# Performance work log

Measured on AMD Instinct MI355X. Metric: run time of the kernel, lower is better.

## Reference

```python
import jax, jax.numpy as jnp
import numpy as np

B, V, CODE_NUM = 64, 100, 4096
CODE_SIZE, ATT, VISIT, TIME, HID, OUT = 256, 128, 256, 64, 512, 90
TYPE_NUM = 32
NEG = -2.0 ** 31


def setup_inputs() -> dict:
    key = jax.random.key(0)
    ks = jax.random.split(key, 24)
    s = 0.02
    return {
        'code_x': jax.random.randint(ks[0], (B, V, CODE_NUM), 0, 2).astype(jnp.float32),
        'code_type0': jax.random.randint(ks[1], (CODE_NUM + 1,), 0, TYPE_NUM),
        'code_type1': jax.random.randint(ks[2], (CODE_NUM + 1,), 0, TYPE_NUM),
        'code_type2': jax.random.randint(ks[3], (CODE_NUM + 1,), 0, TYPE_NUM),
        'lens': jax.random.randint(ks[4], (B,), 1, V + 1),
        'intervals': jax.random.uniform(ks[5], (B, V), dtype=jnp.float32),
        # encoder: code + 3 type embedding tables (rows 1..code_num used)
        'code_emb': jax.random.normal(ks[6], (CODE_NUM + 1, CODE_SIZE), jnp.float32) * s,
        't0_emb': jax.random.normal(ks[7], (TYPE_NUM, CODE_SIZE), jnp.float32) * s,
        't1_emb': jax.random.normal(ks[8], (TYPE_NUM, CODE_SIZE), jnp.float32) * s,
        't2_emb': jax.random.normal(ks[9], (TYPE_NUM, CODE_SIZE), jnp.float32) * s,
        # visit self-attention (no bias, per nn.Linear(..., bias=False))
        'Wq': jax.random.normal(ks[10], (CODE_SIZE, ATT), jnp.float32) * s,
        'Wk': jax.random.normal(ks[11], (CODE_SIZE, ATT), jnp.float32) * s,
        'Wv': jax.random.normal(ks[12], (CODE_SIZE, VISIT), jnp.float32) * s,
        # time embedding Linear(1, time_size)
        'time_w': jax.random.normal(ks[13], (TIME,), jnp.float32) * s,
        'time_b': jnp.zeros((TIME,), jnp.float32),
        # GRUCell params (torch layout: gates ordered r,z,n)
        'gru_Wih': jax.random.normal(ks[14], (3 * HID, VISIT + TIME), jnp.float32) * s,
        'gru_Whh': jax.random.normal(ks[15], (3 * HID, HID), jnp.float32) * s,
        'gru_bih': jnp.zeros((3 * HID,), jnp.float32),
        'gru_bhh': jnp.zeros((3 * HID,), jnp.float32),
        # classifier
        'cls_W': jax.random.normal(ks[16], (OUT, HID), jnp.float32) * s,
        'cls_b': jnp.zeros((OUT,), jnp.float32),
    }


def reference(code_x, code_type0, code_type1, code_type2, lens, intervals,
              code_emb, t0_emb, t1_emb, t2_emb, Wq, Wk, Wv, time_w, time_b,
              gru_Wih, gru_Whh, gru_bih, gru_bhh, cls_W, cls_b):
    # --- Encoder (vectorized): multi-hot slot i corresponds to code id i+1 ---
    E = (code_emb[1:]
         + t0_emb[code_type0[1:]]
         + t1_emb[code_type1[1:]]
         + t2_emb[code_type2[1:]])                      # [CODE_NUM, CODE_SIZE]
    active = (code_x > 0).astype(E.dtype)               # [B, V, CODE_NUM]
    counts = jnp.maximum(active.sum(-1, keepdims=True), 1.0)
    v_emb_ini = jnp.einsum('bvc,cd->bvd', active, E) / counts  # mean over codes
    visit_mask = jnp.arange(V)[None, :] < lens[:, None]        # [B, V]
    v_emb_ini = v_emb_ini * visit_mask[..., None]              # padded visits stay 0

    # --- Context-aware visit self-attention ---
    Q = v_emb_ini @ Wq                                   # [B, V, ATT]
    K = v_emb_ini @ Wk
    Vv = v_emb_ini @ Wv                                  # [B, V, VISIT]
    alpha = jnp.einsum('bqa,bka->bqk', Q, K)
    alpha = jnp.where(visit_mask[:, None, :], alpha, NEG)  # mask keys
    alpha = jax.nn.softmax(alpha, axis=2)
    v_emb = jnp.einsum('bqk,bkd->bqd', alpha, Vv) + Vv     # [B, V, VISIT]

    # --- Time-aware input ---
    t_emb = intervals[..., None] * time_w + time_b         # [B, V, TIME]
    x = jnp.concatenate([v_emb, t_emb], axis=-1)           # [B, V, VISIT+TIME]

    # --- GRU over visits, gated by per-patient length ---
    def step(h, xm):
        xt, mt = xm                                        # xt [B,D], mt [B]
        gi = xt @ gru_Wih.T + gru_bih
        gh = h @ gru_Whh.T + gru_bhh
        ir, iz, inn = jnp.split(gi, 3, axis=-1)
        hr, hz, hn = jnp.split(gh, 3, axis=-1)
        r = jax.nn.sigmoid(ir + hr)
        z = jax.nn.sigmoid(iz + hz)
        n = jnp.tanh(inn + r * hn)
        h_new = (1.0 - z) * n + z * h
        h = jnp.where(mt[:, None], h_new, h)
        return h, None

    h0 = jnp.zeros((B, HID), x.dtype)
    h_final, _ = jax.lax.scan(step, h0, (x.transpose(1, 0, 2), visit_mask.T))

    # --- Classifier (dropout p=0 -> identity) ---
    return jax.nn.sigmoid(h_final @ cls_W.T + cls_b)       # [B, OUT]
```

## Files before the change

kernel.cpp:

```cpp
#include <hip/hip_runtime.h>
#include <hip/hip_bf16.h>

typedef float  f32x4 __attribute__((ext_vector_type(4)));
typedef short  s16x8 __attribute__((ext_vector_type(8)));

#define NEGBIG -1e30f

__device__ __forceinline__ unsigned short f2b(float f) {
    union { float f; unsigned u; } c; c.f = f;
    unsigned r = c.u + 0x7FFF + ((c.u >> 16) & 1);
    return (unsigned short)(r >> 16);
}
__device__ __forceinline__ float b2f(unsigned short h) {
    union { unsigned u; float f; } c; c.u = ((unsigned)h) << 16;
    return c.f;
}
__device__ __forceinline__ float sigm(float x) { return 1.f / (1.f + __expf(-x)); }

__device__ __forceinline__ s16x8 ld_b128_sc(const unsigned short* p) {
    s16x8 r;
    asm volatile("global_load_dwordx4 %0, %1, off sc0 sc1" : "=v"(r) : "v"(p));
    return r;
}
__device__ __forceinline__ void st_short_sc(unsigned short* p, unsigned short v) {
    unsigned int dv = v;
    asm volatile("global_store_short %0, %1, off sc0 sc1" :: "v"(p), "v"(dv) : "memory");
}
__device__ __forceinline__ void st_dword_sc(float* p, float v) {
    asm volatile("global_store_dword %0, %1, off sc0 sc1" :: "v"(p), "v"(v) : "memory");
}

__global__ __launch_bounds__(256) void prep_all(const float* code_emb, const int* ct0, const int* ct1, const int* ct2,
                                                const float* t0e, const float* t1e, const float* t2e,
                                                const float* Wq, const float* Wk, const float* Wv,
                                                const float* gWih, const float* gWhh,
                                                unsigned short* ET, unsigned short* wcat,
                                                unsigned short* wih, unsigned short* whh,
                                                int* flags, unsigned short* hb0) {
    __shared__ float tile[64][65];
    const int bid = blockIdx.x;
    const int t = threadIdx.x;
    if (bid < 256) {
        const int d0 = (bid & 3) * 64, c0 = (bid >> 2) * 64;
        for (int p = 0; p < 16; ++p) {
            int idx = p * 256 + t;
            int dl = idx & 63, cl = idx >> 6;
            int code = c0 + cl + 1;
            int d = d0 + dl;
            float v = code_emb[code * 256 + d] + t0e[ct0[code] * 256 + d]
                    + t1e[ct1[code] * 256 + d] + t2e[ct2[code] * 256 + d];
            tile[dl][cl] = v;
        }
        __syncthreads();
        for (int p = 0; p < 2; ++p) {
            int idx = p * 256 + t;
            int dl = idx >> 3, ch = idx & 7;
            s16x8 pk;
#pragma unroll
            for (int e = 0; e < 8; ++e) pk[e] = (short)f2b(tile[dl][ch * 8 + e]);
            *(s16x8*)(ET + (size_t)(d0 + dl) * 4096 + c0 + ch * 8) = pk;
        }
    } else {
        if (bid >= 504) {
            int idx = (bid - 504) * 256 + t;
            for (int i = idx; i < 1024; i += 2048) flags[i] = 0;
            for (int i = idx; i < 32768; i += 2048) hb0[i] = 0;
        }
        int idx = (bid - 256) * 256 + t;
        const int stride = 256 * 256;
        const int N1 = 131072, N2 = 491520, N3 = 786432;
        for (; idx < N1 + N2 + N3; idx += stride) {
            if (idx < N1) {
                int n = idx >> 8, k = idx & 255;
                float v;
                if (n < 128) v = Wq[k * 128 + n];
                else if (n < 256) v = Wk[k * 128 + (n - 128)];
                else v = Wv[k * 256 + (n - 256)];
                wcat[n * 256 + k] = f2b(v);
            } else if (idx < N1 + N2) {
                int i = idx - N1; wih[i] = f2b(gWih[i]);
            } else {
                int i = idx - N1 - N2; whh[i] = f2b(gWhh[i]);
            }
        }
    }
}

__global__ __launch_bounds__(256) void enc_gemm(const float* code_x, const unsigned short* ET,
                                                const int* lens, unsigned short* Vb) {
    __shared__ __align__(16) char sm[4096 + 32768 + 128];
    char* As = sm;
    char* Bs = sm + 4096;
    float* cl = (float*)(sm + 4096 + 32768);
    const int m0 = blockIdx.x * 32;
    const int t = threadIdx.x, l = t & 63, w = t >> 6;
    const int lr = l & 15, lq = l >> 4, l7 = l & 7;
    const int sr = t >> 3, sc = t & 7;
    const int bn = t >> 3, bc = t & 7;
    const float* gabase = code_x + (size_t)(m0 + sr) * 4096 + sc * 8;
    f32x4 acc[2][4];
#pragma unroll
    for (int a = 0; a < 2; ++a)
#pragma unroll
        for (int b = 0; b < 4; ++b) acc[a][b] = (f32x4){0.f, 0.f, 0.f, 0.f};
    int cnt = 0;

    f32x4 a0A, a1A, a0B, a1B;
    s16x8 bA[8], bB[8];

#define ENC_ISSUE(SLOT, IT) do {                                                     \
    const int k0_ = (IT) * 64;                                                       \
    a0##SLOT = *(const f32x4*)(gabase + k0_);                                        \
    a1##SLOT = *(const f32x4*)(gabase + k0_ + 4);                                    \
    _Pragma("unroll")                                                                \
    for (int rd_ = 0; rd_ < 8; ++rd_)                                                \
        b##SLOT[rd_] = *(const s16x8*)(ET + (size_t)(rd_ * 32 + bn) * 4096 + k0_ + bc * 8); \
} while (0)

#define ENC_CONSUME(SLOT, NEXTIT) do {                                               \
    s16x8 ap_;                                                                       \
    _Pragma("unroll")                                                                \
    for (int e_ = 0; e_ < 4; ++e_) { bool on_ = a0##SLOT[e_] > 0.f; ap_[e_] = on_ ? (short)0x3F80 : (short)0; cnt += on_ ? 1 : 0; } \
    _Pragma("unroll")                                                                \
    for (int e_ = 0; e_ < 4; ++e_) { bool on_ = a1##SLOT[e_] > 0.f; ap_[4 + e_] = on_ ? (short)0x3F80 : (short)0; cnt += on_ ? 1 : 0; } \
    *(s16x8*)(As + sr * 128 + ((sc ^ (sr & 7)) << 4)) = ap_;                         \
    _Pragma("unroll")                                                                \
    for (int rd_ = 0; rd_ < 8; ++rd_) {                                              \
        int n_ = rd_ * 32 + bn;                                                      \
        *(s16x8*)(Bs + n_ * 128 + ((bc ^ (n_ & 7)) << 4)) = b##SLOT[rd_];            \
    }                                                                                \
    if ((NEXTIT) < 64) ENC_ISSUE(SLOT, NEXTIT);                                      \
    __syncthreads();                                                                 \
    _Pragma("unroll")                                                                \
    for (int kk_ = 0; kk_ < 2; ++kk_) {                                              \
        const int cp_ = kk_ * 4 + lq;                                                \
        s16x8 af_[2], bf_[4];                                                        \
        _Pragma("unroll")                                                            \
        for (int mt_ = 0; mt_ < 2; ++mt_)                                            \
            af_[mt_] = *(const s16x8*)(As + (mt_ * 16 + lr) * 128 + ((cp_ ^ l7) << 4)); \
        _Pragma("unroll")                                                            \
        for (int nt_ = 0; nt_ < 4; ++nt_)                                            \
            bf_[nt_] = *(const s16x8*)(Bs + ((w * 4 + nt_) * 16 + lr) * 128 + ((cp_ ^ l7) << 4)); \
        _Pragma("unroll")                                                            \
        for (int mt_ = 0; mt_ < 2; ++mt_)                                            \
            _Pragma("unroll")                                                        \
            for (int nt_ = 0; nt_ < 4; ++nt_)                                        \
                acc[mt_][nt_] = __builtin_amdgcn_mfma_f32_16x16x32_bf16(af_[mt_], bf_[nt_], acc[mt_][nt_], 0, 0, 0); \
    }                                                                                \
    __syncthreads();                                                                 \
} while (0)

    ENC_ISSUE(A, 0);
    ENC_ISSUE(B, 1);
    for (int base = 0; base < 64; base += 2) {
        ENC_CONSUME(A, base + 2);
        ENC_CONSUME(B, base + 3);
    }
#undef ENC_ISSUE
#undef ENC_CONSUME

    float fc = (float)cnt;
    fc += __shfl_xor(fc, 1); fc += __shfl_xor(fc, 2); fc += __shfl_xor(fc, 4);
    if (sc == 0) cl[sr] = fmaxf(fc, 1.f);
    __syncthreads();
#pragma unroll
    for (int mt = 0; mt < 2; ++mt)
#pragma unroll
        for (int i = 0; i < 4; ++i) {
            int m = mt * 16 + lq * 4 + i;
            int gm = m0 + m;
            float rc = 1.f / cl[m];
            unsigned bi = (unsigned)gm / 100u;
            unsigned vi = (unsigned)gm - bi * 100u;
            float msk = ((int)vi < lens[bi]) ? 1.f : 0.f;
#pragma unroll
            for (int nt = 0; nt < 4; ++nt) {
                int n = (w * 4 + nt) * 16 + lr;
                Vb[(size_t)gm * 256 + n] = f2b(acc[mt][nt][i] * rc * msk);
            }
        }
}

__global__ __launch_bounds__(256) void gemm_bf16(const unsigned short* A, const unsigned short* Bm,
                                                 int K, int Ntot, int mode,
                                                 unsigned short* outp, const float* bias) {
    __shared__ __align__(16) char sm[4096 + 32768];
    char* As = sm;
    char* Bs = sm + 4096;
    const int m0 = blockIdx.x * 32;
    const int n0 = blockIdx.y * 256;
    const int t = threadIdx.x, l = t & 63, w = t >> 6;
    const int lr = l & 15, lq = l >> 4, l7 = l & 7;
    const int sr = t >> 3, sc = t & 7;
    const int bn = t >> 3, bc = t & 7;
    const int iters = K >> 6;
    f32x4 acc[2][4];
#pragma unroll
    for (int a = 0; a < 2; ++a)
#pragma unroll
        for (int b = 0; b < 4; ++b) acc[a][b] = (f32x4){0.f, 0.f, 0.f, 0.f};

    s16x8 avA, avB;
    s16x8 bA[8], bB[8];

#define GB_ISSUE(SLOT, IT) do {                                                      \
    const int k0_ = (IT) * 64;                                                       \
    av##SLOT = *(const s16x8*)(A + (size_t)(m0 + sr) * K + k0_ + sc * 8);            \
    _Pragma("unroll")                                                                \
    for (int rd_ = 0; rd_ < 8; ++rd_)                                                \
        b##SLOT[rd_] = *(const s16x8*)(Bm + (size_t)(n0 + rd_ * 32 + bn) * K + k0_ + bc * 8); \
} while (0)

#define GB_CONSUME(SLOT, NEXTIT) do {                                                \
    *(s16x8*)(As + sr * 128 + ((sc ^ (sr & 7)) << 4)) = av##SLOT;                    \
    _Pragma("unroll")                                                                \
    for (int rd_ = 0; rd_ < 8; ++rd_) {                                              \
        int n_ = rd_ * 32 + bn;                                                      \
        *(s16x8*)(Bs + n_ * 128 + ((bc ^ (n_ & 7)) << 4)) = b##SLOT[rd_];            \
    }                                                                                \
    if ((NEXTIT) < iters) GB_ISSUE(SLOT, NEXTIT);                                    \
    __syncthreads();                                                                 \
    _Pragma("unroll")                                                                \
    for (int kk_ = 0; kk_ < 2; ++kk_) {                                              \
        const int cp_ = kk_ * 4 + lq;                                                \
        s16x8 af_[2], bf_[4];                                                        \
        _Pragma("unroll")                                                            \
        for (int mt_ = 0; mt_ < 2; ++mt_)                                            \
            af_[mt_] = *(const s16x8*)(As + (mt_ * 16 + lr) * 128 + ((cp_ ^ l7) << 4)); \
        _Pragma("unroll")                                                            \
        for (int nt_ = 0; nt_ < 4; ++nt_)                                            \
            bf_[nt_] = *(const s16x8*)(Bs + ((w * 4 + nt_) * 16 + lr) * 128 + ((cp_ ^ l7) << 4)); \
        _Pragma("unroll")                                                            \
        for (int mt_ = 0; mt_ < 2; ++mt_)                                            \
            _Pragma("unroll")                                                        \
            for (int nt_ = 0; nt_ < 4; ++nt_)                                        \
                acc[mt_][nt_] = __builtin_amdgcn_mfma_f32_16x16x32_bf16(af_[mt_], bf_[nt_], acc[mt_][nt_], 0, 0, 0); \
    }                                                                                \
    __syncthreads();                                                                 \
} while (0)

    GB_ISSUE(A, 0);
    if (iters > 1) GB_ISSUE(B, 1);
    for (int base = 0; base < iters; base += 2) {
        GB_CONSUME(A, base + 2);
        if (base + 1 < iters) GB_CONSUME(B, base + 3);
    }
#undef GB_ISSUE
#undef GB_CONSUME

#pragma unroll
    for (int mt = 0; mt < 2; ++mt)
#pragma unroll
        for (int i = 0; i < 4; ++i) {
            int gm = m0 + mt * 16 + lq * 4 + i;
#pragma unroll
            for (int nt = 0; nt < 4; ++nt) {
                int n = n0 + (w * 4 + nt) * 16 + lr;
                float v = acc[mt][nt][i];
                if (mode == 1) v += bias[n];
                outp[(size_t)gm * Ntot + n] = f2b(v);
            }
        }
}

__global__ __launch_bounds__(256) void attn_kernel(const unsigned short* QKV, const int* lens,
                                                   const float* intervals, const float* time_w, const float* time_b,
                                                   unsigned short* X) {
    __shared__ __align__(16) char sm[28672 + 32768];
    char* Pb = sm;
    char* VTb = sm + 28672;
    const int b = blockIdx.x;
    const int h = blockIdx.y;
    const int t = threadIdx.x, l = t & 63, w = t >> 6;
    const int lr = l & 15, lq = l >> 4;
    const int lenb = lens[b];
    for (int p = 0; p < 7; ++p) {
        int idx = p * 256 + t;
        *(f32x4*)(Pb + idx * 16) = (f32x4){0.f, 0.f, 0.f, 0.f};
    }
    __syncthreads();
    f32x4 S[2][7];
#pragma unroll
    for (int a = 0; a < 2; ++a)
#pragma unroll
        for (int c = 0; c < 7; ++c) S[a][c] = (f32x4){0.f, 0.f, 0.f, 0.f};
#pragma unroll
    for (int kk = 0; kk < 4; ++kk) {
        s16x8 qa[2], kb[7];
#pragma unroll
        for (int mi = 0; mi < 2; ++mi) {
            int mt = 2 * w + mi;
            if (mt > 6) continue;
            int row = b * 100 + mt * 16 + lr;
            qa[mi] = *(const s16x8*)(QKV + (size_t)row * 512 + kk * 32 + lq * 8);
        }
#pragma unroll
        for (int nt = 0; nt < 7; ++nt) {
            int row = b * 100 + nt * 16 + lr;
            kb[nt] = *(const s16x8*)(QKV + (size_t)row * 512 + 128 + kk * 32 + lq * 8);
        }
#pragma unroll
        for (int mi = 0; mi < 2; ++mi) {
            int mt = 2 * w + mi;
            if (mt > 6) continue;
#pragma unroll
            for (int nt = 0; nt < 7; ++nt)
                S[mi][nt] = __builtin_amdgcn_mfma_f32_16x16x32_bf16(qa[mi], kb[nt], S[mi][nt], 0, 0, 0);
        }
    }
#pragma unroll
    for (int mi = 0; mi < 2; ++mi) {
        int mt = 2 * w + mi;
        if (mt > 6) continue;
        float sv[7][4];
#pragma unroll
        for (int nt = 0; nt < 7; ++nt) {
            int j = nt * 16 + lr;
#pragma unroll
            for (int i = 0; i < 4; ++i)
                sv[nt][i] = (j < lenb) ? S[mi][nt][i] : NEGBIG;
        }
#pragma unroll
        for (int i = 0; i < 4; ++i) {
            float mx = sv[0][i];
#pragma unroll
            for (int nt = 1; nt < 7; ++nt) mx = fmaxf(mx, sv[nt][i]);
            mx = fmaxf(mx, __shfl_xor(mx, 1));
            mx = fmaxf(mx, __shfl_xor(mx, 2));
            mx = fmaxf(mx, __shfl_xor(mx, 4));
            mx = fmaxf(mx, __shfl_xor(mx, 8));
            float e[7], sum = 0.f;
#pragma unroll
            for (int nt = 0; nt < 7; ++nt) { e[nt] = __expf(sv[nt][i] - mx); sum += e[nt]; }
            sum += __shfl_xor(sum, 1);
            sum += __shfl_xor(sum, 2);
            sum += __shfl_xor(sum, 4);
            sum += __shfl_xor(sum, 8);
            float rs = 1.f / sum;
            int m = mt * 16 + lq * 4 + i;
#pragma unroll
            for (int nt = 0; nt < 7; ++nt) {
                int j = nt * 16 + lr;
                *(unsigned short*)(Pb + m * 256 + (((j >> 3) ^ (m & 7)) << 4) + ((j & 7) << 1)) = f2b(e[nt] * rs);
            }
        }
    }
    __syncthreads();
    for (int p = 0; p < 8; ++p) {
        int idx = p * 256 + t;
        *(f32x4*)(VTb + idx * 16) = (f32x4){0.f, 0.f, 0.f, 0.f};
    }
    __syncthreads();
    for (int p = 0; p < 7; ++p) {
        int ci = p * 256 + t;
        if (ci < 1600) {
            int j = ci >> 4, d8 = ci & 15;
            s16x8 vv = *(const s16x8*)(QKV + (size_t)(b * 100 + j) * 512 + 256 + h * 128 + d8 * 8);
#pragma unroll
            for (int e = 0; e < 8; ++e) {
                int dl = d8 * 8 + e;
                *(unsigned short*)(VTb + dl * 256 + (((j >> 3) ^ (dl & 7)) << 4) + ((j & 7) << 1)) = (unsigned short)vv[e];
            }
        }
    }
    __syncthreads();
    f32x4 O[2][8];
#pragma unroll
    for (int a = 0; a < 2; ++a)
#pragma unroll
        for (int c = 0; c < 8; ++c) O[a][c] = (f32x4){0.f, 0.f, 0.f, 0.f};
#pragma unroll
    for (int kk = 0; kk < 4; ++kk) {
        s16x8 pa[2];
#pragma unroll
        for (int mi = 0; mi < 2; ++mi) {
            int mt = 2 * w + mi;
            if (mt > 6) continue;
            int m = mt * 16 + lr;
            pa[mi] = *(const s16x8*)(Pb + m * 256 + (((kk * 4 + lq) ^ (m & 7)) << 4));
        }
#pragma unroll
        for (int nt = 0; nt < 8; ++nt) {
            int dl = nt * 16 + lr;
            s16x8 vb = *(const s16x8*)(VTb + dl * 256 + (((kk * 4 + lq) ^ (dl & 7)) << 4));
#pragma unroll
            for (int mi = 0; mi < 2; ++mi) {
                int mt = 2 * w + mi;
                if (mt > 6) continue;
                O[mi][nt] = __builtin_amdgcn_mfma_f32_16x16x32_bf16(pa[mi], vb, O[mi][nt], 0, 0, 0);
            }
        }
    }
#pragma unroll
    for (int mi = 0; mi < 2; ++mi) {
        int mt = 2 * w + mi;
        if (mt > 6) continue;
#pragma unroll
        for (int i = 0; i < 4; ++i) {
            int m = mt * 16 + lq * 4 + i;
            if (m < 100) {
#pragma unroll
                for (int nt = 0; nt < 8; ++nt) {
                    int dl = nt * 16 + lr;
                    float res = b2f(*(unsigned short*)(VTb + dl * 256 + (((m >> 3) ^ (dl & 7)) << 4) + ((m & 7) << 1)));
                    X[(size_t)(b * 100 + m) * 320 + h * 128 + dl] = f2b(O[mi][nt][i] + res);
                }
            }
        }
    }
    if (h == 0) {
        for (int p = 0; p < 25; ++p) {
            int idx = p * 256 + t;
            int m = idx >> 6, d = idx & 63;
            float val = intervals[b * 100 + m] * time_w[d] + time_b[d];
            X[(size_t)(b * 100 + m) * 320 + 256 + d] = f2b(val);
        }
    }
}

__global__ __launch_bounds__(256, 1) void gru_kernel(const unsigned short* GIb, const unsigned short* WHH,
                                                     const float* gbhh, const int* lens,
                                                     unsigned short* hb0, unsigned short* hb1, float* hf,
                                                     int* flags, const float* clsW, const float* clsb, float* out) {
    const int bid = blockIdx.x;
    const int t = threadIdx.x, l = t & 63, w = t >> 6;
    const int lr = l & 15, lq = l >> 4;
    const int d0 = bid * 16;
    const int j = d0 + lr;
    int ml;
    {
        int v = lens[l];
        v = max(v, __shfl_xor(v, 1));  v = max(v, __shfl_xor(v, 2));
        v = max(v, __shfl_xor(v, 4));  v = max(v, __shfl_xor(v, 8));
        v = max(v, __shfl_xor(v, 16)); v = max(v, __shfl_xor(v, 32));
        ml = v;
    }
    int lens4[4];
#pragma unroll
    for (int i = 0; i < 4; ++i) lens4[i] = lens[w * 16 + lq * 4 + i];
    const float bhr = gbhh[j], bhz = gbhh[512 + j], bhn = gbhh[1024 + j];
    s16x8 Bf[3][16];
#pragma unroll
    for (int g = 0; g < 3; ++g)
#pragma unroll
        for (int kk = 0; kk < 16; ++kk)
            Bf[g][kk] = *(const s16x8*)(WHH + (size_t)(g * 512 + j) * 512 + kk * 32 + lq * 8);
    float ho[4] = {0.f, 0.f, 0.f, 0.f};
    size_t gi_base[4];
#pragma unroll
    for (int i = 0; i < 4; ++i) gi_base[i] = (size_t)((w * 16 + lq * 4 + i) * 100) * 1536 + j;

    float gir[4], giz[4], gin[4];
#pragma unroll
    for (int i = 0; i < 4; ++i) {
        const unsigned short* gp = GIb + gi_base[i];
        gir[i] = b2f(gp[0]); giz[i] = b2f(gp[512]); gin[i] = b2f(gp[1024]);
    }

    for (int step = 0; step < ml; ++step) {
        const unsigned short* hb = (step & 1) ? hb1 : hb0;
        unsigned short* hn = (step & 1) ? hb0 : hb1;
        s16x8 af[16];
#pragma unroll
        for (int kk = 0; kk < 16; ++kk)
            af[kk] = ld_b128_sc(hb + (size_t)(w * 16 + lr) * 512 + kk * 32 + lq * 8);
        asm volatile("s_waitcnt vmcnt(0)" ::: "memory");
        __builtin_amdgcn_sched_barrier(0);
        f32x4 ar = (f32x4){0.f,0.f,0.f,0.f}, az = ar, an = ar;
#pragma unroll
        for (int kk = 0; kk < 16; ++kk) {
            ar = __builtin_amdgcn_mfma_f32_16x16x32_bf16(af[kk], Bf[0][kk], ar, 0, 0, 0);
            az = __builtin_amdgcn_mfma_f32_16x16x32_bf16(af[kk], Bf[1][kk], az, 0, 0, 0);
            an = __builtin_amdgcn_mfma_f32_16x16x32_bf16(af[kk], Bf[2][kk], an, 0, 0, 0);
        }
#pragma unroll
        for (int i = 0; i < 4; ++i) {
            float r = sigm(gir[i] + ar[i] + bhr);
            float z = sigm(giz[i] + az[i] + bhz);
            float n = tanhf(gin[i] + r * (an[i] + bhn));
            float hv = (step < lens4[i]) ? ((1.f - z) * n + z * ho[i]) : ho[i];
            ho[i] = hv;
            st_short_sc(hn + (size_t)(w * 16 + lq * 4 + i) * 512 + j, f2b(hv));
        }
        asm volatile("s_waitcnt vmcnt(0)" ::: "memory");
        __syncthreads();
        if (t == 0)
            __hip_atomic_store(flags + bid * 16, step + 1, __ATOMIC_RELAXED, __HIP_MEMORY_SCOPE_AGENT);
        if (step + 1 < ml) {
#pragma unroll
            for (int i = 0; i < 4; ++i) {
                const unsigned short* gp = GIb + gi_base[i] + (size_t)(step + 1) * 1536;
                gir[i] = b2f(gp[0]); giz[i] = b2f(gp[512]); gin[i] = b2f(gp[1024]);
            }
        }
        if (w == 0) {
            int guard = 0;
            while (true) {
                int v = (l < 32) ? __hip_atomic_load(flags + l * 16, __ATOMIC_RELAXED, __HIP_MEMORY_SCOPE_AGENT) : (step + 1);
                if (__all(v >= step + 1)) break;
                if (++guard > (1 << 20)) break;
                __builtin_amdgcn_s_sleep(1);
            }
        }
        __syncthreads();
    }
#pragma unroll
    for (int i = 0; i < 4; ++i)
        st_dword_sc(hf + (size_t)(w * 16 + lq * 4 + i) * 512 + j, ho[i]);
    asm volatile("s_waitcnt vmcnt(0)" ::: "memory");
    __syncthreads();
    if (t == 0)
        __hip_atomic_store(flags + bid * 16, ml + 1, __ATOMIC_RELAXED, __HIP_MEMORY_SCOPE_AGENT);
    if (w == 0) {
        int guard = 0;
        while (true) {
            int v = (l < 32) ? __hip_atomic_load(flags + l * 16, __ATOMIC_RELAXED, __HIP_MEMORY_SCOPE_AGENT) : (ml + 1);
            if (__all(v >= ml + 1)) break;
            if (++guard > (1 << 20)) break;
            __builtin_amdgcn_s_sleep(1);
        }
    }
    __syncthreads();
    if (bid < 30) {
        int bb = t >> 2, qq = t & 3;
        int c0 = bid * 3;
        float s0 = 0.f, s1 = 0.f, s2 = 0.f;
        for (int kc = 0; kc < 32; ++kc) {
            int k = qq * 128 + kc * 4;
            f32x4 hv = *(const f32x4*)(hf + bb * 512 + k);
            f32x4 w0 = *(const f32x4*)(clsW + (c0 + 0) * 512 + k);
            f32x4 w1 = *(const f32x4*)(clsW + (c0 + 1) * 512 + k);
            f32x4 w2 = *(const f32x4*)(clsW + (c0 + 2) * 512 + k);
            s0 += hv[0] * w0[0] + hv[1] * w0[1] + hv[2] * w0[2] + hv[3] * w0[3];
            s1 += hv[0] * w1[0] + hv[1] * w1[1] + hv[2] * w1[2] + hv[3] * w1[3];
            s2 += hv[0] * w2[0] + hv[1] * w2[1] + hv[2] * w2[2] + hv[3] * w2[3];
        }
        s0 += __shfl_xor(s0, 1); s0 += __shfl_xor(s0, 2);
        s1 += __shfl_xor(s1, 1); s1 += __shfl_xor(s1, 2);
        s2 += __shfl_xor(s2, 1); s2 += __shfl_xor(s2, 2);
        if (qq == 0) {
            out[bb * 90 + c0 + 0] = sigm(s0 + clsb[c0 + 0]);
            out[bb * 90 + c0 + 1] = sigm(s1 + clsb[c0 + 1]);
            out[bb * 90 + c0 + 2] = sigm(s2 + clsb[c0 + 2]);
        }
    }
}

extern "C" void kernel_launch(void* const* d_in, const int* in_sizes, int n_in,
                              void* d_out, int out_size, void* d_ws, size_t ws_size,
                              hipStream_t stream) {
    const float* code_x   = (const float*)d_in[0];
    const int*   ct0      = (const int*)d_in[1];
    const int*   ct1      = (const int*)d_in[2];
    const int*   ct2      = (const int*)d_in[3];
    const int*   lens     = (const int*)d_in[4];
    const float* intervals= (const float*)d_in[5];
    const float* code_emb = (const float*)d_in[6];
    const float* t0e      = (const float*)d_in[7];
    const float* t1e      = (const float*)d_in[8];
    const float* t2e      = (const float*)d_in[9];
    const float* Wq       = (const float*)d_in[10];
    const float* Wk       = (const float*)d_in[11];
    const float* Wv       = (const float*)d_in[12];
    const float* time_w   = (const float*)d_in[13];
    const float* time_b   = (const float*)d_in[14];
    const float* gWih     = (const float*)d_in[15];
    const float* gWhh     = (const float*)d_in[16];
    const float* gbih     = (const float*)d_in[17];
    const float* gbhh     = (const float*)d_in[18];
    const float* clsW     = (const float*)d_in[19];
    const float* clsb     = (const float*)d_in[20];

    char* ws = (char*)d_ws;
    const size_t ET_OFF   = 0;
    const size_t WCAT_OFF = 2097152;
    const size_t WIH_OFF  = 2359296;
    const size_t WHH_OFF  = 3342336;
    const size_t V_OFF    = 4915200;
    const size_t QKV_OFF  = 8192000;
    const size_t X_OFF    = 14778368;
    const size_t GI_OFF   = 18874368;
    const size_t HB0_OFF  = 38535168;
    const size_t HB1_OFF  = 38600704;
    const size_t HF_OFF   = 38666240;
    const size_t FLG_OFF  = 38797312;

    unsigned short* ET   = (unsigned short*)(ws + ET_OFF);
    unsigned short* WCAT = (unsigned short*)(ws + WCAT_OFF);
    unsigned short* WIH  = (unsigned short*)(ws + WIH_OFF);
    unsigned short* WHH  = (unsigned short*)(ws + WHH_OFF);
    unsigned short* Vb   = (unsigned short*)(ws + V_OFF);
    unsigned short* QKV  = (unsigned short*)(ws + QKV_OFF);
    unsigned short* Xb   = (unsigned short*)(ws + X_OFF);
    unsigned short* GIb  = (unsigned short*)(ws + GI_OFF);
    unsigned short* hb0  = (unsigned short*)(ws + HB0_OFF);
    unsigned short* hb1  = (unsigned short*)(ws + HB1_OFF);
    float*          hf   = (float*)(ws + HF_OFF);
    int*            flags= (int*)(ws + FLG_OFF);

    prep_all<<<512, 256, 0, stream>>>(code_emb, ct0, ct1, ct2, t0e, t1e, t2e,
                                      Wq, Wk, Wv, gWih, gWhh,
                                      ET, WCAT, WIH, WHH, flags, hb0);
    enc_gemm<<<200, 256, 0, stream>>>(code_x, ET, lens, Vb);
    gemm_bf16<<<dim3(200, 2), 256, 0, stream>>>(Vb, WCAT, 256, 512, 2, QKV, nullptr);
    attn_kernel<<<dim3(64, 2), 256, 0, stream>>>(QKV, lens, intervals, time_w, time_b, Xb);
    gemm_bf16<<<dim3(200, 6), 256, 0, stream>>>(Xb, WIH, 320, 1536, 1, GIb, gbih);
    gru_kernel<<<32, 256, 0, stream>>>(GIb, WHH, gbhh, lens, hb0, hb1, hf, flags, clsW, clsb, (float*)d_out);
}
```

Baseline: 728.7 us.

## Fuse GRU input projection into the recurrent GRU kernel

Removes the separate GEMM that precomputed the GRU input gates for all timesteps, and the round trip of that result through global memory. Each GRU block now holds its slice of the input weight matrix in registers and computes the next step's input gates with extra MFMAs between the h-state store and the grid barrier. This saves one launch and a large global write/read. The cost is more register pressure, since Wih now stays resident next to Whh, and more MFMA work on the serial recurrence path. There is also a small precision change, because the gates are no longer rounded to bf16.

```diff
diff --git a/kernel.cpp b/kernel.cpp
--- a/kernel.cpp
+++ b/kernel.cpp
@@ -418,7 +418,8 @@
     }
 }
 
-__global__ __launch_bounds__(256, 1) void gru_kernel(const unsigned short* GIb, const unsigned short* WHH,
+__global__ __launch_bounds__(256, 1) void gru_kernel(const unsigned short* Xb, const unsigned short* WHH,
+                                                     const unsigned short* WIH, const float* gbih,
                                                      const float* gbhh, const int* lens,
                                                      unsigned short* hb0, unsigned short* hb1, float* hf,
                                                      int* flags, const float* clsW, const float* clsb, float* out) {
@@ -439,23 +440,42 @@
 #pragma unroll
     for (int i = 0; i < 4; ++i) lens4[i] = lens[w * 16 + lq * 4 + i];
     const float bhr = gbhh[j], bhz = gbhh[512 + j], bhn = gbhh[1024 + j];
+    const float bihr = gbih[j], bihz = gbih[512 + j], bihn = gbih[1024 + j];
     s16x8 Bf[3][16];
 #pragma unroll
     for (int g = 0; g < 3; ++g)
 #pragma unroll
         for (int kk = 0; kk < 16; ++kk)
             Bf[g][kk] = *(const s16x8*)(WHH + (size_t)(g * 512 + j) * 512 + kk * 32 + lq * 8);
+    s16x8 Wi[3][10];
+#pragma unroll
+    for (int g = 0; g < 3; ++g)
+#pragma unroll
+        for (int kk = 0; kk < 10; ++kk)
+            Wi[g][kk] = *(const s16x8*)(WIH + (size_t)(g * 512 + j) * 320 + kk * 32 + lq * 8);
     float ho[4] = {0.f, 0.f, 0.f, 0.f};
-    size_t gi_base[4];
-#pragma unroll
-    for (int i = 0; i < 4; ++i) gi_base[i] = (size_t)((w * 16 + lq * 4 + i) * 100) * 1536 + j;
+    const size_t xbase = ((size_t)(w * 16 + lr) * 100) * 320 + lq * 8;
 
     float gir[4], giz[4], gin[4];
-#pragma unroll
-    for (int i = 0; i < 4; ++i) {
-        const unsigned short* gp = GIb + gi_base[i];
-        gir[i] = b2f(gp[0]); giz[i] = b2f(gp[512]); gin[i] = b2f(gp[1024]);
-    }
+#define GI_COMPUTE(S) do {                                                           \
+    s16x8 xa_[10];                                                                   \
+    _Pragma("unroll")                                                                \
+    for (int kk_ = 0; kk_ < 10; ++kk_)                                               \
+        xa_[kk_] = *(const s16x8*)(Xb + xbase + (size_t)(S) * 320 + kk_ * 32);       \
+    f32x4 gr_ = (f32x4){0.f,0.f,0.f,0.f}, gz_ = gr_, gn_ = gr_;                      \
+    _Pragma("unroll")                                                                \
+    for (int kk_ = 0; kk_ < 10; ++kk_) {                                             \
+        gr_ = __builtin_amdgcn_mfma_f32_16x16x32_bf16(xa_[kk_], Wi[0][kk_], gr_, 0, 0, 0); \
+        gz_ = __builtin_amdgcn_mfma_f32_16x16x32_bf16(xa_[kk_], Wi[1][kk_], gz_, 0, 0, 0); \
+        gn_ = __builtin_amdgcn_mfma_f32_16x16x32_bf16(xa_[kk_], Wi[2][kk_], gn_, 0, 0, 0); \
+    }                                                                                \
+    _Pragma("unroll")                                                                \
+    for (int i_ = 0; i_ < 4; ++i_) {                                                 \
+        gir[i_] = gr_[i_] + bihr; giz[i_] = gz_[i_] + bihz; gin[i_] = gn_[i_] + bihn; \
+    }                                                                                \
+} while (0)
+
+    GI_COMPUTE(0);
 
     for (int step = 0; step < ml; ++step) {
         const unsigned short* hb = (step & 1) ? hb1 : hb0;
@@ -487,11 +507,7 @@
         if (t == 0)
             __hip_atomic_store(flags + bid * 16, step + 1, __ATOMIC_RELAXED, __HIP_MEMORY_SCOPE_AGENT);
         if (step + 1 < ml) {
-#pragma unroll
-            for (int i = 0; i < 4; ++i) {
-                const unsigned short* gp = GIb + gi_base[i] + (size_t)(step + 1) * 1536;
-                gir[i] = b2f(gp[0]); giz[i] = b2f(gp[512]); gin[i] = b2f(gp[1024]);
-            }
+            GI_COMPUTE(step + 1);
         }
         if (w == 0) {
             int guard = 0;
@@ -504,6 +520,7 @@
         }
         __syncthreads();
     }
+#undef GI_COMPUTE
 #pragma unroll
     for (int i = 0; i < 4; ++i)
         st_dword_sc(hf + (size_t)(w * 16 + lq * 4 + i) * 512 + j, ho[i]);
@@ -579,7 +596,6 @@
     const size_t V_OFF    = 4915200;
     const size_t QKV_OFF  = 8192000;
     const size_t X_OFF    = 14778368;
-    const size_t GI_OFF   = 18874368;
     const size_t HB0_OFF  = 38535168;
     const size_t HB1_OFF  = 38600704;
     const size_t HF_OFF   = 38666240;
@@ -592,7 +608,6 @@
     unsigned short* Vb   = (unsigned short*)(ws + V_OFF);
     unsigned short* QKV  = (unsigned short*)(ws + QKV_OFF);
     unsigned short* Xb   = (unsigned short*)(ws + X_OFF);
-    unsigned short* GIb  = (unsigned short*)(ws + GI_OFF);
     unsigned short* hb0  = (unsigned short*)(ws + HB0_OFF);
     unsigned short* hb1  = (unsigned short*)(ws + HB1_OFF);
     float*          hf   = (float*)(ws + HF_OFF);
@@ -604,6 +619,5 @@
     enc_gemm<<<200, 256, 0, stream>>>(code_x, ET, lens, Vb);
     gemm_bf16<<<dim3(200, 2), 256, 0, stream>>>(Vb, WCAT, 256, 512, 2, QKV, nullptr);
     attn_kernel<<<dim3(64, 2), 256, 0, stream>>>(QKV, lens, intervals, time_w, time_b, Xb);
-    gemm_bf16<<<dim3(200, 6), 256, 0, stream>>>(Xb, WIH, 320, 1536, 1, GIb, gbih);
-    gru_kernel<<<32, 256, 0, stream>>>(GIb, WHH, gbhh, lens, hb0, hb1, hf, flags, clsW, clsb, (float*)d_out);
-}
+    gru_kernel<<<32, 256, 0, stream>>>(Xb, WHH, WIH, gbih, gbhh, lens, hb0, hb1, hf, flags, clsW, clsb, (float*)d_out);
+}
```

Result: slower. 838.7 us (+15.1%).
